# Performance work log

Hardware: AMD Instinct MI355X
Metric: run time of the kernel (lower is better)

Reference implementation:

```python
import jax, jax.numpy as jnp
import numpy as np

N = 50000   # nodes
E = 800000  # edges (avg degree 16)
D = 128     # in = hidden = out feats


def setup_inputs() -> dict:
    key = jax.random.key(0)
    ks = jax.random.split(key, 9)
    x = jax.random.normal(ks[0], (N, D), dtype=jnp.float32)
    edge_index = jax.random.randint(ks[1], (2, E), 0, N, dtype=jnp.int64)
    s = 1.0 / np.sqrt(D)
    # SAGEConv layer 0 (128 -> 128): lin_l (aggregated neighbors, with bias), lin_r (root, no bias)
    Wl0 = jax.random.uniform(ks[2], (D, D), jnp.float32, -s, s)
    Wr0 = jax.random.uniform(ks[3], (D, D), jnp.float32, -s, s)
    b0 = jax.random.uniform(ks[4], (D,), jnp.float32, -s, s)
    # SAGEConv layer 1 (128 -> 128)
    Wl1 = jax.random.uniform(ks[5], (D, D), jnp.float32, -s, s)
    Wr1 = jax.random.uniform(ks[6], (D, D), jnp.float32, -s, s)
    b1 = jax.random.uniform(ks[7], (D,), jnp.float32, -s, s)
    return {"x": x, "edge_index": edge_index,
            "Wl0": Wl0, "Wr0": Wr0, "b0": b0,
            "Wl1": Wl1, "Wr1": Wr1, "b1": b1}


def _sage_conv(x, src, dst, Wl, Wr, b):
    # mean aggregation of neighbor messages x[src] into dst nodes
    msgs = x[src]                                                    # [E, D]
    summed = jax.ops.segment_sum(msgs, dst, num_segments=N)         # [N, D]
    deg = jax.ops.segment_sum(jnp.ones((src.shape[0], 1), x.dtype), dst,
                              num_segments=N)                       # [N, 1]
    agg = summed / jnp.maximum(deg, 1.0)
    # out = lin_l(agg) + lin_r(x); only lin_l has bias (PyG default)
    return agg @ Wl.T + b + x @ Wr.T


def reference(x, edge_index, Wl0, Wr0, b0, Wl1, Wr1, b1):
    src, dst = edge_index[0], edge_index[1]
    h = jax.nn.relu(_sage_conv(x, src, dst, Wl0, Wr0, b0))
    out = _sage_conv(h, src, dst, Wl1, Wr1, b1)  # no ReLU on last layer
    return out
```

## Files before the change

kernel.cpp:

```cpp
#include <hip/hip_runtime.h>


#define D 128
#define NBITS 7
#define BNODES 128
#define GA 64
typedef unsigned short u16;
typedef unsigned u32;
typedef short bf16x8 __attribute__((ext_vector_type(8)));
typedef float f32x4 __attribute__((ext_vector_type(4)));

__device__ __forceinline__ u16 f2bf(float f) {
    union { float f; unsigned u; } x;
    x.f = f;
    unsigned r = x.u + 0x7FFF + ((x.u >> 16) & 1);
    return (u16)(r >> 16);
}
__device__ __forceinline__ float bf2f(u16 b) {
    union { unsigned u; float f; } x;
    x.u = ((unsigned)b) << 16;
    return x.f;
}


__global__ __launch_bounds__(1024) void bucket_hist(const int* __restrict__ dst,
                                                    int* __restrict__ Gcounts,
                                                    int E, int NB, int chunk) {
    __shared__ int cnt[512];
    for (int i = threadIdx.x; i < NB; i += 1024) cnt[i] = 0;
    __syncthreads();
    int base = blockIdx.x * chunk;
    int end = base + chunk; if (end > E) end = E;
    for (int e = base + threadIdx.x; e < end; e += 1024)
        atomicAdd(&cnt[dst[e] >> NBITS], 1);
    __syncthreads();
    for (int b = threadIdx.x; b < NB; b += 1024)
        Gcounts[b * GA + blockIdx.x] = cnt[b];
}

__global__ __launch_bounds__(1024) void scan1_kernel(const int* __restrict__ in,
                                                     int* __restrict__ excl,
                                                     int* __restrict__ totals, int n) {
    int chunk = blockIdx.x;
    int i = chunk * 1024 + threadIdx.x;
    int v = (i < n) ? in[i] : 0;
    int lane = threadIdx.x & 63;
    int wid = threadIdx.x >> 6;
    int s = v;
    #pragma unroll
    for (int off = 1; off < 64; off <<= 1) {
        int t = __shfl_up(s, off);
        if (lane >= off) s += t;
    }
    __shared__ int wsum[16];
    if (lane == 63) wsum[wid] = s;
    __syncthreads();
    if (wid == 0) {
        int ws = (lane < 16) ? wsum[lane] : 0;
        #pragma unroll
        for (int off = 1; off < 16; off <<= 1) {
            int t = __shfl_up(ws, off);
            if (lane >= off) ws += t;
        }
        if (lane < 16) wsum[lane] = ws;
    }
    __syncthreads();
    int wave_off = (wid > 0) ? wsum[wid - 1] : 0;
    int incl = s + wave_off;
    if (i < n) excl[i] = incl - v;
    if (threadIdx.x == 1023) totals[chunk] = incl;
}

__global__ __launch_bounds__(1024) void scan_add(int* __restrict__ Sc,
                                                 const int* __restrict__ totals, int n) {
    int chunk = blockIdx.x;
    int i = chunk * 1024 + threadIdx.x;
    int off = 0;
    for (int j = 0; j < chunk; ++j) off += totals[j];
    if (i < n) Sc[i] += off;
}

__global__ __launch_bounds__(1024) void bucket_scatter(const int* __restrict__ src,
                                                       const int* __restrict__ dst,
                                                       const int* __restrict__ Sc,
                                                       u32* __restrict__ Ebuck,
                                                       int E, int NB, int chunk) {
    __shared__ int cur[512];
    for (int b = threadIdx.x; b < NB; b += 1024) cur[b] = Sc[b * GA + blockIdx.x];
    __syncthreads();
    int base = blockIdx.x * chunk;
    int end = base + chunk; if (end > E) end = E;
    for (int e = base + threadIdx.x; e < end; e += 1024) {
        int d = dst[e];
        int b = d >> NBITS;
        int pos = atomicAdd(&cur[b], 1);
        Ebuck[pos] = ((u32)(d & (BNODES - 1)) << 16) | (u32)src[e];
    }
}

__global__ __launch_bounds__(256) void bucket_sort_csr(u32* __restrict__ Ebuck,
                                                       const int* __restrict__ Sc,
                                                       int* __restrict__ row_ptr,
                                                       int E, int N, int NB) {
    __shared__ int hist[BNODES], excl[BNODES], cur[BNODES];
    __shared__ u16 sorted[8192];
    int b = blockIdx.x;
    int start = Sc[b * GA];
    int endv = (b + 1 < NB) ? Sc[(b + 1) * GA] : E;
    int cnt = endv - start;
    if (cnt > 8192) cnt = 8192;
    for (int i = threadIdx.x; i < BNODES; i += 256) hist[i] = 0;
    __syncthreads();
    for (int i = threadIdx.x; i < cnt; i += 256)
        atomicAdd(&hist[Ebuck[start + i] >> 16], 1);
    __syncthreads();
    if (threadIdx.x == 0) {
        int run = 0;
        for (int i = 0; i < BNODES; ++i) { excl[i] = run; run += hist[i]; }
    }
    __syncthreads();
    for (int i = threadIdx.x; i < BNODES; i += 256) {
        cur[i] = excl[i];
        int g = b * BNODES + i;
        if (g <= N) row_ptr[g] = start + excl[i];
    }
    __syncthreads();
    for (int i = threadIdx.x; i < cnt; i += 256) {
        u32 r = Ebuck[start + i];
        int pos = atomicAdd(&cur[r >> 16], 1);
        sorted[pos] = (u16)(r & 0xFFFF);
    }
    __syncthreads();
    for (int i = threadIdx.x; i < cnt; i += 256)
        ((int*)Ebuck)[start + i] = (int)sorted[i];
}

__global__ void f32_to_bf16_kernel(const float* __restrict__ in, u16* __restrict__ out, int n4) {
    int i = blockIdx.x * 256 + threadIdx.x;
    if (i < n4) {
        float4 v = *(const float4*)&in[i * 4];
        ushort4 o;
        o.x = f2bf(v.x); o.y = f2bf(v.y); o.z = f2bf(v.z); o.w = f2bf(v.w);
        *(ushort4*)&out[i * 4] = o;
    }
}

__global__ void convert_weights(const float* __restrict__ w0, const float* __restrict__ w1,
                                const float* __restrict__ w2, const float* __restrict__ w3,
                                u16* __restrict__ o0, u16* __restrict__ o1,
                                u16* __restrict__ o2, u16* __restrict__ o3) {
    int i = blockIdx.x * 256 + threadIdx.x;
    const int q = D * D / 4;
    int m = i / q, j = i % q;
    const float* in = (m == 0) ? w0 : (m == 1) ? w1 : (m == 2) ? w2 : w3;
    u16* out = (m == 0) ? o0 : (m == 1) ? o1 : (m == 2) ? o2 : o3;
    float4 v = *(const float4*)&in[j * 4];
    ushort4 o;
    o.x = f2bf(v.x); o.y = f2bf(v.y); o.z = f2bf(v.z); o.w = f2bf(v.w);
    *(ushort4*)&out[j * 4] = o;
}

__global__ __launch_bounds__(256) void aggregate_bf16(const u16* __restrict__ xb,
                                                      const int* __restrict__ row_ptr,
                                                      const int* __restrict__ csr,
                                                      u16* __restrict__ aggb, int n) {
    int node = blockIdx.x * 4 + (threadIdx.x >> 6);
    if (node >= n) return;
    int lane = threadIdx.x & 63;
    int half = lane >> 5;
    int fl = (lane & 31) * 4;
    int begin = row_ptr[node], end = row_ptr[node + 1];
    float a0 = 0.f, a1 = 0.f, a2 = 0.f, a3 = 0.f;
    int j = begin + half;
    for (; j + 2 < end; j += 4) {
        int s0 = csr[j], s1 = csr[j + 2];
        ushort4 v0 = *(const ushort4*)&xb[s0 * D + fl];
        ushort4 v1 = *(const ushort4*)&xb[s1 * D + fl];
        a0 += bf2f(v0.x) + bf2f(v1.x);
        a1 += bf2f(v0.y) + bf2f(v1.y);
        a2 += bf2f(v0.z) + bf2f(v1.z);
        a3 += bf2f(v0.w) + bf2f(v1.w);
    }
    if (j < end) {
        int s0 = csr[j];
        ushort4 v0 = *(const ushort4*)&xb[s0 * D + fl];
        a0 += bf2f(v0.x); a1 += bf2f(v0.y); a2 += bf2f(v0.z); a3 += bf2f(v0.w);
    }
    a0 += __shfl_xor(a0, 32);
    a1 += __shfl_xor(a1, 32);
    a2 += __shfl_xor(a2, 32);
    a3 += __shfl_xor(a3, 32);
    if (half == 0) {
        int d = end - begin;
        if (d < 1) d = 1;
        float inv = 1.0f / (float)d;
        ushort4 o;
        o.x = f2bf(a0 * inv); o.y = f2bf(a1 * inv);
        o.z = f2bf(a2 * inv); o.w = f2bf(a3 * inv);
        *(ushort4*)&aggb[node * D + fl] = o;
    }
}

#define LSTR 136

__global__ __launch_bounds__(256) void gemm_mfma(const u16* __restrict__ Aroot,
                                                 const u16* __restrict__ Wr,
                                                 const u16* __restrict__ Agg,
                                                 const u16* __restrict__ Wl,
                                                 const float* __restrict__ bias,
                                                 void* __restrict__ out,
                                                 int n, int mode) {
    __shared__ __align__(16) u16 Lr[64 * LSTR];
    __shared__ __align__(16) u16 Lg[64 * LSTR];
    const int tid = threadIdx.x;
    const int n0 = blockIdx.x * 64;

    {
        int row = tid >> 4;
        int c = (tid & 15) * 8;
        #pragma unroll
        for (int p = 0; p < 4; ++p) {
            int r = p * 16 + row;
            int g = n0 + r;
            float4 vr = make_float4(0.f, 0.f, 0.f, 0.f);
            float4 vg = make_float4(0.f, 0.f, 0.f, 0.f);
            if (g < n) {
                vr = *(const float4*)&Aroot[g * D + c];
                vg = *(const float4*)&Agg[g * D + c];
            }
            *(float4*)&Lr[r * LSTR + c] = vr;
            *(float4*)&Lg[r * LSTR + c] = vg;
        }
    }

    const int wave = tid >> 6;
    const int lane = tid & 63;
    const int quad = lane >> 4;
    const int l16 = lane & 15;

    bf16x8 wr[2][4], wl[2][4];
    #pragma unroll
    for (int mt = 0; mt < 2; ++mt) {
        int jrow = wave * 32 + mt * 16 + l16;
        #pragma unroll
        for (int kb = 0; kb < 4; ++kb) {
            wr[mt][kb] = *(const bf16x8*)&Wr[jrow * D + kb * 32 + quad * 8];
            wl[mt][kb] = *(const bf16x8*)&Wl[jrow * D + kb * 32 + quad * 8];
        }
    }

    __syncthreads();

    f32x4 acc[4][2];
    #pragma unroll
    for (int it = 0; it < 4; ++it)
        #pragma unroll
        for (int mt = 0; mt < 2; ++mt)
            acc[it][mt] = (f32x4){0.f, 0.f, 0.f, 0.f};

    #pragma unroll
    for (int it = 0; it < 4; ++it) {
        int base = (it * 16 + l16) * LSTR + quad * 8;
        #pragma unroll
        for (int kb = 0; kb < 4; ++kb) {
            bf16x8 bx = *(const bf16x8*)&Lr[base + kb * 32];
            bf16x8 bg = *(const bf16x8*)&Lg[base + kb * 32];
            #pragma unroll
            for (int mt = 0; mt < 2; ++mt) {
                acc[it][mt] = __builtin_amdgcn_mfma_f32_16x16x32_bf16(wr[mt][kb], bx, acc[it][mt], 0, 0, 0);
                acc[it][mt] = __builtin_amdgcn_mfma_f32_16x16x32_bf16(wl[mt][kb], bg, acc[it][mt], 0, 0, 0);
            }
        }
    }

    #pragma unroll
    for (int it = 0; it < 4; ++it) {
        int i = n0 + it * 16 + l16;
        if (i < n) {
            #pragma unroll
            for (int mt = 0; mt < 2; ++mt) {
                int j0 = wave * 32 + mt * 16 + quad * 4;
                float4 bv = *(const float4*)&bias[j0];
                float o0 = acc[it][mt][0] + bv.x;
                float o1 = acc[it][mt][1] + bv.y;
                float o2 = acc[it][mt][2] + bv.z;
                float o3 = acc[it][mt][3] + bv.w;
                if (mode) {
                    o0 = fmaxf(o0, 0.f); o1 = fmaxf(o1, 0.f);
                    o2 = fmaxf(o2, 0.f); o3 = fmaxf(o3, 0.f);
                    ushort4 ob;
                    ob.x = f2bf(o0); ob.y = f2bf(o1); ob.z = f2bf(o2); ob.w = f2bf(o3);
                    *(ushort4*)&((u16*)out)[i * D + j0] = ob;
                } else {
                    float4 of = make_float4(o0, o1, o2, o3);
                    *(float4*)&((float*)out)[i * D + j0] = of;
                }
            }
        }
    }
}


extern "C" void kernel_launch(void* const* d_in, const int* in_sizes, int n_in,
                              void* d_out, int out_size, void* d_ws, size_t ws_size,
                              hipStream_t stream) {
    const float* x = (const float*)d_in[0];
    const int* edge = (const int*)d_in[1];
    const float* Wl0 = (const float*)d_in[2];
    const float* Wr0 = (const float*)d_in[3];
    const float* b0 = (const float*)d_in[4];
    const float* Wl1 = (const float*)d_in[5];
    const float* Wr1 = (const float*)d_in[6];
    const float* b1 = (const float*)d_in[7];

    const int N = in_sizes[0] / D;
    const int E = in_sizes[1] / 2;
    const int* src = edge;
    const int* dst = edge + E;

    char* ws = (char*)d_ws;
    size_t off = 0;
    auto alloc = [&](size_t bytes) {
        char* p = ws + off;
        off += (bytes + 255) & ~(size_t)255;
        return p;
    };
    int* row_ptr = (int*)alloc((size_t)(N + 1) * 4);
    u32* Ebuck = (u32*)alloc((size_t)E * 4);
    u16* xb = (u16*)alloc((size_t)N * D * 2);
    u16* hb = (u16*)alloc((size_t)N * D * 2);
    u16* aggb = (u16*)alloc((size_t)N * D * 2);
    u16* Wl0b = (u16*)alloc((size_t)D * D * 2);
    u16* Wr0b = (u16*)alloc((size_t)D * D * 2);
    u16* Wl1b = (u16*)alloc((size_t)D * D * 2);
    u16* Wr1b = (u16*)alloc((size_t)D * D * 2);
    const int NB = (N + BNODES - 1) / BNODES;
    const int scanN = NB * GA;
    int* Gcounts = (int*)aggb;
    int* Sc = Gcounts + scanN;
    int* totals = Sc + scanN;

    (void)ws_size; (void)n_in; (void)out_size;

    const int chunk = (E + GA - 1) / GA;
    const int scanBlocks = (scanN + 1023) / 1024;

    bucket_hist<<<GA, 1024, 0, stream>>>(dst, Gcounts, E, NB, chunk);
    scan1_kernel<<<scanBlocks, 1024, 0, stream>>>(Gcounts, Sc, totals, scanN);
    scan_add<<<scanBlocks, 1024, 0, stream>>>(Sc, totals, scanN);
    bucket_scatter<<<GA, 1024, 0, stream>>>(src, dst, Sc, Ebuck, E, NB, chunk);
    bucket_sort_csr<<<NB, 256, 0, stream>>>(Ebuck, Sc, row_ptr, E, N, NB);
    const int* csr = (const int*)Ebuck;

    int xQuads = N * D / 4;
    f32_to_bf16_kernel<<<(xQuads + 255) / 256, 256, 0, stream>>>(x, xb, xQuads);
    convert_weights<<<(4 * D * D / 4 + 255) / 256, 256, 0, stream>>>(
        Wl0, Wr0, Wl1, Wr1, Wl0b, Wr0b, Wl1b, Wr1b);

    int aggBlocks = (N + 3) / 4;
    int gemmBlocks = (N + 63) / 64;

    aggregate_bf16<<<aggBlocks, 256, 0, stream>>>(xb, row_ptr, csr, aggb, N);
    gemm_mfma<<<gemmBlocks, 256, 0, stream>>>(xb, Wr0b, aggb, Wl0b, b0, hb, N, 1);
    aggregate_bf16<<<aggBlocks, 256, 0, stream>>>(hb, row_ptr, csr, aggb, N);
    gemm_mfma<<<gemmBlocks, 256, 0, stream>>>(hb, Wr1b, aggb, Wl1b, b1, d_out, N, 0);
}
```

Before: 228.8 us.

## Fuse neighbor aggregation into MFMA layer kernel and consolidate CSR preprocessing launches

Neighbor mean aggregation is moved into the GEMM kernel: each wave gathers 16 nodes' neighbor rows straight into shared memory, so the aggregated bf16 tensor is never written to or re-read from global memory. Preprocessing is also consolidated. Histogram and the x/weight bf16 conversions share one launch, and the two-pass scan becomes a single-block scan. CSR indices are stored as 16-bit values in their own buffer. The trade-off is that the gather now runs serially per wave over 16 nodes with far fewer waves in flight than the old standalone aggregation kernel, which may expose memory latency.

New measurement: 277.3 us. +21.2%, slower.

```diff
diff --git a/kernel.cpp b/kernel.cpp
--- a/kernel.cpp
+++ b/kernel.cpp
@@ -22,38 +22,66 @@
     return x.f;
 }
 
-
-__global__ __launch_bounds__(1024) void bucket_hist(const int* __restrict__ dst,
-                                                    int* __restrict__ Gcounts,
-                                                    int E, int NB, int chunk) {
-    __shared__ int cnt[512];
-    for (int i = threadIdx.x; i < NB; i += 1024) cnt[i] = 0;
-    __syncthreads();
-    int base = blockIdx.x * chunk;
-    int end = base + chunk; if (end > E) end = E;
-    for (int e = base + threadIdx.x; e < end; e += 1024)
-        atomicAdd(&cnt[dst[e] >> NBITS], 1);
-    __syncthreads();
-    for (int b = threadIdx.x; b < NB; b += 1024)
-        Gcounts[b * GA + blockIdx.x] = cnt[b];
-}
-
-__global__ __launch_bounds__(1024) void scan1_kernel(const int* __restrict__ in,
-                                                     int* __restrict__ excl,
-                                                     int* __restrict__ totals, int n) {
-    int chunk = blockIdx.x;
-    int i = chunk * 1024 + threadIdx.x;
-    int v = (i < n) ? in[i] : 0;
+__global__ __launch_bounds__(1024) void hist_and_convert(
+        const int* __restrict__ dst, int* __restrict__ Gcounts, int E, int NB, int chunk,
+        const float* __restrict__ x, u16* __restrict__ xb, int xQuads,
+        const float* __restrict__ w0, const float* __restrict__ w1,
+        const float* __restrict__ w2, const float* __restrict__ w3,
+        u16* __restrict__ o0, u16* __restrict__ o1,
+        u16* __restrict__ o2, u16* __restrict__ o3) {
+    if (blockIdx.x < GA) {
+        __shared__ int cnt[512];
+        for (int i = threadIdx.x; i < NB; i += 1024) cnt[i] = 0;
+        __syncthreads();
+        int base = blockIdx.x * chunk;
+        int end = base + chunk; if (end > E) end = E;
+        for (int e = base + threadIdx.x; e < end; e += 1024)
+            atomicAdd(&cnt[dst[e] >> NBITS], 1);
+        __syncthreads();
+        for (int b = threadIdx.x; b < NB; b += 1024)
+            Gcounts[b * GA + blockIdx.x] = cnt[b];
+    } else {
+        int i = (blockIdx.x - GA) * 1024 + threadIdx.x;
+        if (i < xQuads) {
+            float4 v = *(const float4*)&x[i * 4];
+            ushort4 o;
+            o.x = f2bf(v.x); o.y = f2bf(v.y); o.z = f2bf(v.z); o.w = f2bf(v.w);
+            *(ushort4*)&xb[i * 4] = o;
+        } else {
+            int j = i - xQuads;
+            const int q = D * D / 4;
+            if (j < 4 * q) {
+                int m = j / q, k = j % q;
+                const float* in = (m == 0) ? w0 : (m == 1) ? w1 : (m == 2) ? w2 : w3;
+                u16* op = (m == 0) ? o0 : (m == 1) ? o1 : (m == 2) ? o2 : o3;
+                float4 v = *(const float4*)&in[k * 4];
+                ushort4 o;
+                o.x = f2bf(v.x); o.y = f2bf(v.y); o.z = f2bf(v.z); o.w = f2bf(v.w);
+                *(ushort4*)&op[k * 4] = o;
+            }
+        }
+    }
+}
+
+__global__ __launch_bounds__(1024) void scan_single(const int* __restrict__ in,
+                                                    int* __restrict__ out, int n) {
+    int CH = (n + 1023) >> 10;
+    int base = threadIdx.x * CH;
+    int s = 0;
+    for (int k = 0; k < CH; ++k) {
+        int i = base + k;
+        if (i < n) s += in[i];
+    }
     int lane = threadIdx.x & 63;
     int wid = threadIdx.x >> 6;
-    int s = v;
+    int ps = s;
     #pragma unroll
     for (int off = 1; off < 64; off <<= 1) {
-        int t = __shfl_up(s, off);
-        if (lane >= off) s += t;
+        int t = __shfl_up(ps, off);
+        if (lane >= off) ps += t;
     }
     __shared__ int wsum[16];
-    if (lane == 63) wsum[wid] = s;
+    if (lane == 63) wsum[wid] = ps;
     __syncthreads();
     if (wid == 0) {
         int ws = (lane < 16) ? wsum[lane] : 0;
@@ -65,19 +93,11 @@
         if (lane < 16) wsum[lane] = ws;
     }
     __syncthreads();
-    int wave_off = (wid > 0) ? wsum[wid - 1] : 0;
-    int incl = s + wave_off;
-    if (i < n) excl[i] = incl - v;
-    if (threadIdx.x == 1023) totals[chunk] = incl;
-}
-
-__global__ __launch_bounds__(1024) void scan_add(int* __restrict__ Sc,
-                                                 const int* __restrict__ totals, int n) {
-    int chunk = blockIdx.x;
-    int i = chunk * 1024 + threadIdx.x;
-    int off = 0;
-    for (int j = 0; j < chunk; ++j) off += totals[j];
-    if (i < n) Sc[i] += off;
+    int run = (ps - s) + ((wid > 0) ? wsum[wid - 1] : 0);
+    for (int k = 0; k < CH; ++k) {
+        int i = base + k;
+        if (i < n) { int v = in[i]; out[i] = run; run += v; }
+    }
 }
 
 __global__ __launch_bounds__(1024) void bucket_scatter(const int* __restrict__ src,
@@ -98,9 +118,10 @@
     }
 }
 
-__global__ __launch_bounds__(256) void bucket_sort_csr(u32* __restrict__ Ebuck,
+__global__ __launch_bounds__(256) void bucket_sort_csr(const u32* __restrict__ Ebuck,
                                                        const int* __restrict__ Sc,
                                                        int* __restrict__ row_ptr,
+                                                       u16* __restrict__ csr,
                                                        int E, int N, int NB) {
     __shared__ int hist[BNODES], excl[BNODES], cur[BNODES];
     __shared__ u16 sorted[8192];
@@ -132,84 +153,19 @@
     }
     __syncthreads();
     for (int i = threadIdx.x; i < cnt; i += 256)
-        ((int*)Ebuck)[start + i] = (int)sorted[i];
-}
-
-__global__ void f32_to_bf16_kernel(const float* __restrict__ in, u16* __restrict__ out, int n4) {
-    int i = blockIdx.x * 256 + threadIdx.x;
-    if (i < n4) {
-        float4 v = *(const float4*)&in[i * 4];
-        ushort4 o;
-        o.x = f2bf(v.x); o.y = f2bf(v.y); o.z = f2bf(v.z); o.w = f2bf(v.w);
-        *(ushort4*)&out[i * 4] = o;
-    }
-}
-
-__global__ void convert_weights(const float* __restrict__ w0, const float* __restrict__ w1,
-                                const float* __restrict__ w2, const float* __restrict__ w3,
-                                u16* __restrict__ o0, u16* __restrict__ o1,
-                                u16* __restrict__ o2, u16* __restrict__ o3) {
-    int i = blockIdx.x * 256 + threadIdx.x;
-    const int q = D * D / 4;
-    int m = i / q, j = i % q;
-    const float* in = (m == 0) ? w0 : (m == 1) ? w1 : (m == 2) ? w2 : w3;
-    u16* out = (m == 0) ? o0 : (m == 1) ? o1 : (m == 2) ? o2 : o3;
-    float4 v = *(const float4*)&in[j * 4];
-    ushort4 o;
-    o.x = f2bf(v.x); o.y = f2bf(v.y); o.z = f2bf(v.z); o.w = f2bf(v.w);
-    *(ushort4*)&out[j * 4] = o;
-}
-
-__global__ __launch_bounds__(256) void aggregate_bf16(const u16* __restrict__ xb,
-                                                      const int* __restrict__ row_ptr,
-                                                      const int* __restrict__ csr,
-                                                      u16* __restrict__ aggb, int n) {
-    int node = blockIdx.x * 4 + (threadIdx.x >> 6);
-    if (node >= n) return;
-    int lane = threadIdx.x & 63;
-    int half = lane >> 5;
-    int fl = (lane & 31) * 4;
-    int begin = row_ptr[node], end = row_ptr[node + 1];
-    float a0 = 0.f, a1 = 0.f, a2 = 0.f, a3 = 0.f;
-    int j = begin + half;
-    for (; j + 2 < end; j += 4) {
-        int s0 = csr[j], s1 = csr[j + 2];
-        ushort4 v0 = *(const ushort4*)&xb[s0 * D + fl];
-        ushort4 v1 = *(const ushort4*)&xb[s1 * D + fl];
-        a0 += bf2f(v0.x) + bf2f(v1.x);
-        a1 += bf2f(v0.y) + bf2f(v1.y);
-        a2 += bf2f(v0.z) + bf2f(v1.z);
-        a3 += bf2f(v0.w) + bf2f(v1.w);
-    }
-    if (j < end) {
-        int s0 = csr[j];
-        ushort4 v0 = *(const ushort4*)&xb[s0 * D + fl];
-        a0 += bf2f(v0.x); a1 += bf2f(v0.y); a2 += bf2f(v0.z); a3 += bf2f(v0.w);
-    }
-    a0 += __shfl_xor(a0, 32);
-    a1 += __shfl_xor(a1, 32);
-    a2 += __shfl_xor(a2, 32);
-    a3 += __shfl_xor(a3, 32);
-    if (half == 0) {
-        int d = end - begin;
-        if (d < 1) d = 1;
-        float inv = 1.0f / (float)d;
-        ushort4 o;
-        o.x = f2bf(a0 * inv); o.y = f2bf(a1 * inv);
-        o.z = f2bf(a2 * inv); o.w = f2bf(a3 * inv);
-        *(ushort4*)&aggb[node * D + fl] = o;
-    }
+        csr[start + i] = sorted[i];
 }
 
 #define LSTR 136
 
-__global__ __launch_bounds__(256) void gemm_mfma(const u16* __restrict__ Aroot,
-                                                 const u16* __restrict__ Wr,
-                                                 const u16* __restrict__ Agg,
-                                                 const u16* __restrict__ Wl,
-                                                 const float* __restrict__ bias,
-                                                 void* __restrict__ out,
-                                                 int n, int mode) {
+__global__ __launch_bounds__(256) void sage_layer(const u16* __restrict__ A,
+                                                  const int* __restrict__ row_ptr,
+                                                  const u16* __restrict__ csr,
+                                                  const u16* __restrict__ Wr,
+                                                  const u16* __restrict__ Wl,
+                                                  const float* __restrict__ bias,
+                                                  void* __restrict__ out,
+                                                  int n, int mode) {
     __shared__ __align__(16) u16 Lr[64 * LSTR];
     __shared__ __align__(16) u16 Lg[64 * LSTR];
     const int tid = threadIdx.x;
@@ -223,21 +179,56 @@
             int r = p * 16 + row;
             int g = n0 + r;
             float4 vr = make_float4(0.f, 0.f, 0.f, 0.f);
-            float4 vg = make_float4(0.f, 0.f, 0.f, 0.f);
-            if (g < n) {
-                vr = *(const float4*)&Aroot[g * D + c];
-                vg = *(const float4*)&Agg[g * D + c];
-            }
+            if (g < n) vr = *(const float4*)&A[g * D + c];
             *(float4*)&Lr[r * LSTR + c] = vr;
-            *(float4*)&Lg[r * LSTR + c] = vg;
         }
     }
 
     const int wave = tid >> 6;
     const int lane = tid & 63;
+    const int half = lane >> 5;
+    const int fl = (lane & 31) * 4;
+
+    for (int t = 0; t < 16; ++t) {
+        int r = wave * 16 + t;
+        int node = n0 + r;
+        float a0 = 0.f, a1 = 0.f, a2 = 0.f, a3 = 0.f;
+        int begin = 0, end = 0;
+        if (node < n) { begin = row_ptr[node]; end = row_ptr[node + 1]; }
+        int j = begin + half;
+        for (; j + 6 < end; j += 8) {
+            int s0 = csr[j], s1 = csr[j + 2], s2 = csr[j + 4], s3 = csr[j + 6];
+            ushort4 v0 = *(const ushort4*)&A[s0 * D + fl];
+            ushort4 v1 = *(const ushort4*)&A[s1 * D + fl];
+            ushort4 v2 = *(const ushort4*)&A[s2 * D + fl];
+            ushort4 v3 = *(const ushort4*)&A[s3 * D + fl];
+            a0 += (bf2f(v0.x) + bf2f(v1.x)) + (bf2f(v2.x) + bf2f(v3.x));
+            a1 += (bf2f(v0.y) + bf2f(v1.y)) + (bf2f(v2.y) + bf2f(v3.y));
+            a2 += (bf2f(v0.z) + bf2f(v1.z)) + (bf2f(v2.z) + bf2f(v3.z));
+            a3 += (bf2f(v0.w) + bf2f(v1.w)) + (bf2f(v2.w) + bf2f(v3.w));
+        }
+        for (; j < end; j += 2) {
+            int s0 = csr[j];
+            ushort4 v0 = *(const ushort4*)&A[s0 * D + fl];
+            a0 += bf2f(v0.x); a1 += bf2f(v0.y); a2 += bf2f(v0.z); a3 += bf2f(v0.w);
+        }
+        a0 += __shfl_xor(a0, 32);
+        a1 += __shfl_xor(a1, 32);
+        a2 += __shfl_xor(a2, 32);
+        a3 += __shfl_xor(a3, 32);
+        if (half == 0) {
+            int d = end - begin;
+            if (d < 1) d = 1;
+            float inv = 1.0f / (float)d;
+            ushort4 o;
+            o.x = f2bf(a0 * inv); o.y = f2bf(a1 * inv);
+            o.z = f2bf(a2 * inv); o.w = f2bf(a3 * inv);
+            *(ushort4*)&Lg[r * LSTR + fl] = o;
+        }
+    }
+
     const int quad = lane >> 4;
     const int l16 = lane & 15;
-
     bf16x8 wr[2][4], wl[2][4];
     #pragma unroll
     for (int mt = 0; mt < 2; ++mt) {
@@ -327,41 +318,34 @@
     };
     int* row_ptr = (int*)alloc((size_t)(N + 1) * 4);
     u32* Ebuck = (u32*)alloc((size_t)E * 4);
+    u16* csrb = (u16*)alloc((size_t)E * 2);
     u16* xb = (u16*)alloc((size_t)N * D * 2);
     u16* hb = (u16*)alloc((size_t)N * D * 2);
-    u16* aggb = (u16*)alloc((size_t)N * D * 2);
     u16* Wl0b = (u16*)alloc((size_t)D * D * 2);
     u16* Wr0b = (u16*)alloc((size_t)D * D * 2);
     u16* Wl1b = (u16*)alloc((size_t)D * D * 2);
     u16* Wr1b = (u16*)alloc((size_t)D * D * 2);
     const int NB = (N + BNODES - 1) / BNODES;
     const int scanN = NB * GA;
-    int* Gcounts = (int*)aggb;
-    int* Sc = Gcounts + scanN;
-    int* totals = Sc + scanN;
+    int* Gcounts = (int*)alloc((size_t)scanN * 4);
+    int* Sc = (int*)alloc((size_t)scanN * 4);
 
     (void)ws_size; (void)n_in; (void)out_size;
 
     const int chunk = (E + GA - 1) / GA;
-    const int scanBlocks = (scanN + 1023) / 1024;
-
-    bucket_hist<<<GA, 1024, 0, stream>>>(dst, Gcounts, E, NB, chunk);
-    scan1_kernel<<<scanBlocks, 1024, 0, stream>>>(Gcounts, Sc, totals, scanN);
-    scan_add<<<scanBlocks, 1024, 0, stream>>>(Sc, totals, scanN);
+    const int xQuads = N * D / 4;
+    const int convQuads = xQuads + 4 * D * D / 4;
+    const int histGrid = GA + (convQuads + 1023) / 1024;
+    const int gemmBlocks = (N + 63) / 64;
+
+    hist_and_convert<<<histGrid, 1024, 0, stream>>>(
+        dst, Gcounts, E, NB, chunk,
+        x, xb, xQuads,
+        Wl0, Wr0, Wl1, Wr1, Wl0b, Wr0b, Wl1b, Wr1b);
+    scan_single<<<1, 1024, 0, stream>>>(Gcounts, Sc, scanN);
     bucket_scatter<<<GA, 1024, 0, stream>>>(src, dst, Sc, Ebuck, E, NB, chunk);
-    bucket_sort_csr<<<NB, 256, 0, stream>>>(Ebuck, Sc, row_ptr, E, N, NB);
-    const int* csr = (const int*)Ebuck;
-
-    int xQuads = N * D / 4;
-    f32_to_bf16_kernel<<<(xQuads + 255) / 256, 256, 0, stream>>>(x, xb, xQuads);
-    convert_weights<<<(4 * D * D / 4 + 255) / 256, 256, 0, stream>>>(
-        Wl0, Wr0, Wl1, Wr1, Wl0b, Wr0b, Wl1b, Wr1b);
-
-    int aggBlocks = (N + 3) / 4;
-    int gemmBlocks = (N + 63) / 64;
-
-    aggregate_bf16<<<aggBlocks, 256, 0, stream>>>(xb, row_ptr, csr, aggb, N);
-    gemm_mfma<<<gemmBlocks, 256, 0, stream>>>(xb, Wr0b, aggb, Wl0b, b0, hb, N, 1);
-    aggregate_bf16<<<aggBlocks, 256, 0, stream>>>(hb, row_ptr, csr, aggb, N);
-    gemm_mfma<<<gemmBlocks, 256, 0, stream>>>(hb, Wr1b, aggb, Wl1b, b1, d_out, N, 0);
-}
+    bucket_sort_csr<<<NB, 256, 0, stream>>>(Ebuck, Sc, row_ptr, csrb, E, N, NB);
+
+    sage_layer<<<gemmBlocks, 256, 0, stream>>>(xb, row_ptr, csrb, Wr0b, Wl0b, b0, hb, N, 1);
+    sage_layer<<<gemmBlocks, 256, 0, stream>>>(hb, row_ptr, csrb, Wr1b, Wl1b, b1, d_out, N, 0);
+}
```

## Fuse histogram with bf16 conversion, fold scan-add into consumers, store CSR as u16

Applied to the files above, without the earlier changes.

Merges the bucket histogram and the x/weight bf16 conversion into a single launch, using a block-index split. Removes the scan_add kernel by having bucket_scatter and bucket_sort_csr each recompute per-chunk offsets from the totals with a wave scan. Stores the CSR source indices as 16-bit values, which halves index traffic in both aggregation passes. Together this cuts three kernel launches, at the cost of a heavier fused kernel, redundant offset scans per block, and a dependence on N fitting in 16 bits.

After: 218.9 us. -4.3%, faster.

```diff
diff --git a/kernel.cpp b/kernel.cpp
--- a/kernel.cpp
+++ b/kernel.cpp
@@ -22,20 +22,45 @@
     return x.f;
 }
 
-
-__global__ __launch_bounds__(1024) void bucket_hist(const int* __restrict__ dst,
-                                                    int* __restrict__ Gcounts,
-                                                    int E, int NB, int chunk) {
-    __shared__ int cnt[512];
-    for (int i = threadIdx.x; i < NB; i += 1024) cnt[i] = 0;
-    __syncthreads();
-    int base = blockIdx.x * chunk;
-    int end = base + chunk; if (end > E) end = E;
-    for (int e = base + threadIdx.x; e < end; e += 1024)
-        atomicAdd(&cnt[dst[e] >> NBITS], 1);
-    __syncthreads();
-    for (int b = threadIdx.x; b < NB; b += 1024)
-        Gcounts[b * GA + blockIdx.x] = cnt[b];
+__global__ __launch_bounds__(1024) void hist_and_convert(
+        const int* __restrict__ dst, int* __restrict__ Gcounts, int E, int NB, int chunk,
+        const float* __restrict__ x, u16* __restrict__ xb, int xQuads,
+        const float* __restrict__ w0, const float* __restrict__ w1,
+        const float* __restrict__ w2, const float* __restrict__ w3,
+        u16* __restrict__ o0, u16* __restrict__ o1,
+        u16* __restrict__ o2, u16* __restrict__ o3) {
+    if (blockIdx.x < GA) {
+        __shared__ int cnt[512];
+        for (int i = threadIdx.x; i < NB; i += 1024) cnt[i] = 0;
+        __syncthreads();
+        int base = blockIdx.x * chunk;
+        int end = base + chunk; if (end > E) end = E;
+        for (int e = base + threadIdx.x; e < end; e += 1024)
+            atomicAdd(&cnt[dst[e] >> NBITS], 1);
+        __syncthreads();
+        for (int b = threadIdx.x; b < NB; b += 1024)
+            Gcounts[b * GA + blockIdx.x] = cnt[b];
+    } else {
+        int i = (blockIdx.x - GA) * 1024 + threadIdx.x;
+        if (i < xQuads) {
+            float4 v = *(const float4*)&x[i * 4];
+            ushort4 o;
+            o.x = f2bf(v.x); o.y = f2bf(v.y); o.z = f2bf(v.z); o.w = f2bf(v.w);
+            *(ushort4*)&xb[i * 4] = o;
+        } else {
+            int j = i - xQuads;
+            const int q = D * D / 4;
+            if (j < 4 * q) {
+                int m = j / q, k = j % q;
+                const float* in = (m == 0) ? w0 : (m == 1) ? w1 : (m == 2) ? w2 : w3;
+                u16* op = (m == 0) ? o0 : (m == 1) ? o1 : (m == 2) ? o2 : o3;
+                float4 v = *(const float4*)&in[k * 4];
+                ushort4 o;
+                o.x = f2bf(v.x); o.y = f2bf(v.y); o.z = f2bf(v.z); o.w = f2bf(v.w);
+                *(ushort4*)&op[k * 4] = o;
+            }
+        }
+    }
 }
 
 __global__ __launch_bounds__(1024) void scan1_kernel(const int* __restrict__ in,
@@ -71,22 +96,35 @@
     if (threadIdx.x == 1023) totals[chunk] = incl;
 }
 
-__global__ __launch_bounds__(1024) void scan_add(int* __restrict__ Sc,
-                                                 const int* __restrict__ totals, int n) {
-    int chunk = blockIdx.x;
-    int i = chunk * 1024 + threadIdx.x;
-    int off = 0;
-    for (int j = 0; j < chunk; ++j) off += totals[j];
-    if (i < n) Sc[i] += off;
+__device__ __forceinline__ void load_choff(const int* __restrict__ totals,
+                                           int nChunks, int* choff) {
+    if (threadIdx.x < 64) {
+        int t = threadIdx.x;
+        int v = (t < nChunks) ? totals[t] : 0;
+        int s = v;
+        #pragma unroll
+        for (int off = 1; off < 64; off <<= 1) {
+            int u = __shfl_up(s, off);
+            if (t >= off) s += u;
+        }
+        if (t < 32) choff[t] = s - v;
+    }
 }
 
 __global__ __launch_bounds__(1024) void bucket_scatter(const int* __restrict__ src,
                                                        const int* __restrict__ dst,
-                                                       const int* __restrict__ Sc,
+                                                       const int* __restrict__ excl,
+                                                       const int* __restrict__ totals,
                                                        u32* __restrict__ Ebuck,
-                                                       int E, int NB, int chunk) {
+                                                       int E, int NB, int chunk, int nChunks) {
     __shared__ int cur[512];
-    for (int b = threadIdx.x; b < NB; b += 1024) cur[b] = Sc[b * GA + blockIdx.x];
+    __shared__ int choff[32];
+    load_choff(totals, nChunks, choff);
+    __syncthreads();
+    for (int b = threadIdx.x; b < NB; b += 1024) {
+        int idx = b * GA + blockIdx.x;
+        cur[b] = excl[idx] + choff[idx >> 10];
+    }
     __syncthreads();
     int base = blockIdx.x * chunk;
     int end = base + chunk; if (end > E) end = E;
@@ -98,15 +136,25 @@
     }
 }
 
-__global__ __launch_bounds__(256) void bucket_sort_csr(u32* __restrict__ Ebuck,
-                                                       const int* __restrict__ Sc,
+__global__ __launch_bounds__(256) void bucket_sort_csr(const u32* __restrict__ Ebuck,
+                                                       const int* __restrict__ excl_g,
+                                                       const int* __restrict__ totals,
                                                        int* __restrict__ row_ptr,
-                                                       int E, int N, int NB) {
+                                                       u16* __restrict__ csr,
+                                                       int E, int N, int NB, int nChunks) {
     __shared__ int hist[BNODES], excl[BNODES], cur[BNODES];
     __shared__ u16 sorted[8192];
+    __shared__ int choff[32];
+    load_choff(totals, nChunks, choff);
+    __syncthreads();
     int b = blockIdx.x;
-    int start = Sc[b * GA];
-    int endv = (b + 1 < NB) ? Sc[(b + 1) * GA] : E;
+    int idx0 = b * GA;
+    int start = excl_g[idx0] + choff[idx0 >> 10];
+    int endv = E;
+    if (b + 1 < NB) {
+        int idx1 = (b + 1) * GA;
+        endv = excl_g[idx1] + choff[idx1 >> 10];
+    }
     int cnt = endv - start;
     if (cnt > 8192) cnt = 8192;
     for (int i = threadIdx.x; i < BNODES; i += 256) hist[i] = 0;
@@ -132,37 +180,12 @@
     }
     __syncthreads();
     for (int i = threadIdx.x; i < cnt; i += 256)
-        ((int*)Ebuck)[start + i] = (int)sorted[i];
-}
-
-__global__ void f32_to_bf16_kernel(const float* __restrict__ in, u16* __restrict__ out, int n4) {
-    int i = blockIdx.x * 256 + threadIdx.x;
-    if (i < n4) {
-        float4 v = *(const float4*)&in[i * 4];
-        ushort4 o;
-        o.x = f2bf(v.x); o.y = f2bf(v.y); o.z = f2bf(v.z); o.w = f2bf(v.w);
-        *(ushort4*)&out[i * 4] = o;
-    }
-}
-
-__global__ void convert_weights(const float* __restrict__ w0, const float* __restrict__ w1,
-                                const float* __restrict__ w2, const float* __restrict__ w3,
-                                u16* __restrict__ o0, u16* __restrict__ o1,
-                                u16* __restrict__ o2, u16* __restrict__ o3) {
-    int i = blockIdx.x * 256 + threadIdx.x;
-    const int q = D * D / 4;
-    int m = i / q, j = i % q;
-    const float* in = (m == 0) ? w0 : (m == 1) ? w1 : (m == 2) ? w2 : w3;
-    u16* out = (m == 0) ? o0 : (m == 1) ? o1 : (m == 2) ? o2 : o3;
-    float4 v = *(const float4*)&in[j * 4];
-    ushort4 o;
-    o.x = f2bf(v.x); o.y = f2bf(v.y); o.z = f2bf(v.z); o.w = f2bf(v.w);
-    *(ushort4*)&out[j * 4] = o;
+        csr[start + i] = sorted[i];
 }
 
 __global__ __launch_bounds__(256) void aggregate_bf16(const u16* __restrict__ xb,
                                                       const int* __restrict__ row_ptr,
-                                                      const int* __restrict__ csr,
+                                                      const u16* __restrict__ csr,
                                                       u16* __restrict__ aggb, int n) {
     int node = blockIdx.x * 4 + (threadIdx.x >> 6);
     if (node >= n) return;
@@ -327,6 +350,7 @@
     };
     int* row_ptr = (int*)alloc((size_t)(N + 1) * 4);
     u32* Ebuck = (u32*)alloc((size_t)E * 4);
+    u16* csrb = (u16*)alloc((size_t)E * 2);
     u16* xb = (u16*)alloc((size_t)N * D * 2);
     u16* hb = (u16*)alloc((size_t)N * D * 2);
     u16* aggb = (u16*)alloc((size_t)N * D * 2);
@@ -336,32 +360,30 @@
     u16* Wr1b = (u16*)alloc((size_t)D * D * 2);
     const int NB = (N + BNODES - 1) / BNODES;
     const int scanN = NB * GA;
-    int* Gcounts = (int*)aggb;
-    int* Sc = Gcounts + scanN;
-    int* totals = Sc + scanN;
+    int* Gcounts = (int*)alloc((size_t)scanN * 4);
+    int* Sc = (int*)alloc((size_t)scanN * 4);
+    int* totals = (int*)alloc(32 * 4);
 
     (void)ws_size; (void)n_in; (void)out_size;
 
     const int chunk = (E + GA - 1) / GA;
-    const int scanBlocks = (scanN + 1023) / 1024;
-
-    bucket_hist<<<GA, 1024, 0, stream>>>(dst, Gcounts, E, NB, chunk);
-    scan1_kernel<<<scanBlocks, 1024, 0, stream>>>(Gcounts, Sc, totals, scanN);
-    scan_add<<<scanBlocks, 1024, 0, stream>>>(Sc, totals, scanN);
-    bucket_scatter<<<GA, 1024, 0, stream>>>(src, dst, Sc, Ebuck, E, NB, chunk);
-    bucket_sort_csr<<<NB, 256, 0, stream>>>(Ebuck, Sc, row_ptr, E, N, NB);
-    const int* csr = (const int*)Ebuck;
-
-    int xQuads = N * D / 4;
-    f32_to_bf16_kernel<<<(xQuads + 255) / 256, 256, 0, stream>>>(x, xb, xQuads);
-    convert_weights<<<(4 * D * D / 4 + 255) / 256, 256, 0, stream>>>(
+    const int xQuads = N * D / 4;
+    const int convQuads = xQuads + 4 * D * D / 4;
+    const int histGrid = GA + (convQuads + 1023) / 1024;
+    const int nChunks = (scanN + 1023) / 1024;
+    const int aggBlocks = (N + 3) / 4;
+    const int gemmBlocks = (N + 63) / 64;
+
+    hist_and_convert<<<histGrid, 1024, 0, stream>>>(
+        dst, Gcounts, E, NB, chunk,
+        x, xb, xQuads,
         Wl0, Wr0, Wl1, Wr1, Wl0b, Wr0b, Wl1b, Wr1b);
-
-    int aggBlocks = (N + 3) / 4;
-    int gemmBlocks = (N + 63) / 64;
-
-    aggregate_bf16<<<aggBlocks, 256, 0, stream>>>(xb, row_ptr, csr, aggb, N);
+    scan1_kernel<<<nChunks, 1024, 0, stream>>>(Gcounts, Sc, totals, scanN);
+    bucket_scatter<<<GA, 1024, 0, stream>>>(src, dst, Sc, totals, Ebuck, E, NB, chunk, nChunks);
+    bucket_sort_csr<<<NB, 256, 0, stream>>>(Ebuck, Sc, totals, row_ptr, csrb, E, N, NB, nChunks);
+
+    aggregate_bf16<<<aggBlocks, 256, 0, stream>>>(xb, row_ptr, csrb, aggb, N);
     gemm_mfma<<<gemmBlocks, 256, 0, stream>>>(xb, Wr0b, aggb, Wl0b, b0, hb, N, 1);
-    aggregate_bf16<<<aggBlocks, 256, 0, stream>>>(hb, row_ptr, csr, aggb, N);
+    aggregate_bf16<<<aggBlocks, 256, 0, stream>>>(hb, row_ptr, csrb, aggb, N);
     gemm_mfma<<<gemmBlocks, 256, 0, stream>>>(hb, Wr1b, aggb, Wl1b, b1, d_out, N, 0);
 }
```
